# Performance work log

Hardware: AMD Instinct MI355X
Metric: run time of the kernel (lower is better)

Reference implementation:

```python
import jax, jax.numpy as jnp
import numpy as np

N_NODES = 100000
N_EDGES = 1600000
IN_F, HID_F, OUT_F = 128, 128, 128


def setup_inputs() -> dict:
    key = jax.random.key(0)
    k1, k2, k3, k4, k5, k6 = jax.random.split(key, 6)
    x = jax.random.normal(k1, (N_NODES, IN_F), dtype=jnp.float32)
    edge_index = jax.random.randint(k2, (2, N_EDGES), 0, N_NODES, dtype=jnp.int32)
    # nn.Linear params (PyTorch layout: W [out, in], y = x @ W.T + b)
    s1 = 1.0 / np.sqrt(IN_F)
    W1 = jax.random.uniform(k3, (HID_F, IN_F), minval=-s1, maxval=s1, dtype=jnp.float32)
    b1 = jax.random.uniform(k4, (HID_F,), minval=-s1, maxval=s1, dtype=jnp.float32)
    s2 = 1.0 / np.sqrt(HID_F)
    W2 = jax.random.uniform(k5, (OUT_F, HID_F), minval=-s2, maxval=s2, dtype=jnp.float32)
    b2 = jax.random.uniform(k6, (OUT_F,), minval=-s2, maxval=s2, dtype=jnp.float32)
    return {"x": x, "edge_index": edge_index, "W1": W1, "b1": b1, "W2": W2, "b2": b2}


def _spmm_mean(h, row, col, deg_inv):
    # (adj @ h)[i] = sum_{edges e: row[e]==i} h[col[e]], then scale by deg_inv[i]
    agg = jax.ops.segment_sum(h[col], row, num_segments=N_NODES)
    return agg * deg_inv[:, None]


def reference(x, edge_index, W1, b1, W2, b2):
    row, col = edge_index[0], edge_index[1]
    # degree = row-sum of adjacency (duplicates in COO are summed, matching torch)
    deg = jax.ops.segment_sum(jnp.ones((N_EDGES,), dtype=x.dtype), row, num_segments=N_NODES)
    deg_inv = jnp.where(deg > 0, 1.0 / deg, 0.0)
    # dropout in eval mode = identity
    h = x @ W1.T + b1
    h = _spmm_mean(h, row, col, deg_inv)
    h = jax.nn.elu(h)
    h = h @ W2.T + b2
    h = _spmm_mean(h, row, col, deg_inv)
    return h
```

## Files before the change

kernel.cpp:

```cpp
#include <hip/hip_runtime.h>
#include <math.h>

#define N_NODES 100000
#define N_EDGES 1600000
#define F 128
#define NBUCK 196
#define EPB 4096
#define CAP 9216

typedef _Float16 f16x2 __attribute__((ext_vector_type(2)));
typedef _Float16 f16x8 __attribute__((ext_vector_type(8)));
typedef __fp16 fp16x2 __attribute__((ext_vector_type(2)));
typedef float f32x2 __attribute__((ext_vector_type(2)));
typedef float f32x4 __attribute__((ext_vector_type(4)));

__device__ inline uint pkrtz(float a, float b) {
    union { fp16x2 h; uint u; } c;
    c.h = __builtin_amdgcn_cvt_pkrtz(a, b);
    return c.u;
}
__device__ inline f16x2 as2(uint u) {
    union { uint u; f16x2 h; } c; c.u = u; return c.h;
}

__device__ inline int wave_incl_scan(int v, int lane) {
#pragma unroll
    for (int off = 1; off < 64; off <<= 1) {
        int t = __shfl_up(v, off);
        if (lane >= off) v += t;
    }
    return v;
}


__global__ __launch_bounds__(256) void bucketize_kernel(const int* __restrict__ row,
                                                        const int* __restrict__ col,
                                                        int* __restrict__ bucket_cursor,
                                                        int* __restrict__ pairs) {
    __shared__ int stage[EPB];
    __shared__ unsigned char bid[EPB];
    __shared__ int lcnt[NBUCK], lcur[NBUCK], loff[NBUCK], gbase[NBUCK];
    __shared__ int wsum[4];
    const int tid = threadIdx.x;
    const int lane = tid & 63;
    const int wid = tid >> 6;
    const int base = blockIdx.x * EPB;
    const int cnt = min(N_EDGES - base, EPB);

    for (int i = tid; i < NBUCK; i += 256) { lcnt[i] = 0; lcur[i] = 0; }
    __syncthreads();
    for (int i = 0; i < EPB / 256; ++i) {
        int e = base + i * 256 + tid;
        if (e < N_EDGES) atomicAdd(&lcnt[row[e] >> 9], 1);
    }
    __syncthreads();
    {
        int v = (tid < NBUCK) ? lcnt[tid] : 0;
        int inc = wave_incl_scan(v, lane);
        if (lane == 63) wsum[wid] = inc;
        __syncthreads();
        if (tid == 0) {
            int a = 0;
#pragma unroll
            for (int i = 0; i < 4; ++i) { int t = wsum[i]; wsum[i] = a; a += t; }
        }
        __syncthreads();
        if (tid < NBUCK) loff[tid] = inc - v + wsum[wid];
    }
    if (tid < NBUCK) {
        int c = lcnt[tid];
        gbase[tid] = c ? atomicAdd(&bucket_cursor[tid], c) : 0;
    }
    __syncthreads();
    for (int i = 0; i < EPB / 256; ++i) {
        int e = base + i * 256 + tid;
        if (e < N_EDGES) {
            int r = row[e], c = col[e];
            int b = r >> 9;
            int rk = atomicAdd(&lcur[b], 1);
            int q = loff[b] + rk;
            stage[q] = ((r & 511) << 17) | c;
            bid[q] = (unsigned char)b;
        }
    }
    __syncthreads();
    for (int q = tid; q < cnt; q += 256) {
        int b = bid[q];
        int t = gbase[b] + (q - loff[b]);
        if (t < CAP) pairs[b * CAP + t] = stage[q];
    }
}

__global__ __launch_bounds__(512) void csr_finalize_kernel(const int* __restrict__ pairs,
                                                           const int* __restrict__ bucket_cursor,
                                                           int* __restrict__ csr_col,
                                                           int2* __restrict__ rs,
                                                           float* __restrict__ deg_inv) {
    __shared__ int rcnt[512], rcnt2[512], roff[512];
    __shared__ int colstage[CAP];
    __shared__ int wsum[8];
    const int tid = threadIdx.x;
    const int lane = tid & 63;
    const int wid = tid >> 6;
    const int b = blockIdx.x;
    const int cnt = min(bucket_cursor[b], CAP);
    const int base = b * CAP;
    const int* reg = &pairs[base];

    rcnt[tid] = 0;
    rcnt2[tid] = 0;
    __syncthreads();
    for (int q = tid; q < cnt; q += 512) atomicAdd(&rcnt[reg[q] >> 17], 1);
    __syncthreads();
    const int d = rcnt[tid];
    int inc = wave_incl_scan(d, lane);
    if (lane == 63) wsum[wid] = inc;
    __syncthreads();
    if (tid == 0) {
        int a = 0;
#pragma unroll
        for (int i = 0; i < 8; ++i) { int t = wsum[i]; wsum[i] = a; a += t; }
    }
    __syncthreads();
    const int excl = inc - d + wsum[wid];
    roff[tid] = excl;
    const int grow = (b << 9) + tid;
    if (grow < N_NODES) {
        rs[grow] = make_int2(base + excl, d);
        deg_inv[grow] = d ? 1.0f / (float)d : 0.0f;
    }
    __syncthreads();
    for (int q = tid; q < cnt; q += 512) {
        int v = reg[q];
        int lr = v >> 17;
        int rk = atomicAdd(&rcnt2[lr], 1);
        colstage[roff[lr] + rk] = v & 0x1FFFF;
    }
    __syncthreads();
    for (int q = tid; q < cnt; q += 512) csr_col[base + q] = colstage[q];
}


__global__ __launch_bounds__(256) void convert_w_kernel(const float* __restrict__ W1,
                                                        const float* __restrict__ W2,
                                                        uint* __restrict__ W1h,
                                                        uint* __restrict__ W2h) {
    int i = blockIdx.x * 256 + threadIdx.x;
    if (i < F * F / 2) {
        float2 a = *(const float2*)&W1[i * 2];
        float2 b = *(const float2*)&W2[i * 2];
        W1h[i] = pkrtz(a.x, a.y);
        W2h[i] = pkrtz(b.x, b.y);
    }
}


template <bool IN_F16>
__global__ __launch_bounds__(256, 4) void gemm_mfma_kernel(const void* __restrict__ Xv,
                                                           const ushort* __restrict__ Wh,
                                                           const float* __restrict__ bias,
                                                           ushort* __restrict__ Y) {
    __shared__ __align__(16) char smraw[4 * 16 * 132 * 4];
    ushort* xs = (ushort*)smraw;
    float (*ys)[16][132] = (float(*)[16][132])smraw;

    const int tid = threadIdx.x;
    const int m0 = blockIdx.x << 6;

    if (!IN_F16) {
        const float* X = (const float*)Xv;
        for (int i = 0; i < 8; ++i) {
            int f = i * 256 + tid;
            int r = f >> 5, c = f & 31;
            int gr = m0 + r; gr = gr < N_NODES ? gr : N_NODES - 1;
            float4 v = *(const float4*)&X[(size_t)gr * F + (c << 2)];
            uint2 o = {pkrtz(v.x, v.y), pkrtz(v.z, v.w)};
            *(uint2*)&xs[r * 136 + (c << 2)] = o;
        }
    } else {
        const ushort* X = (const ushort*)Xv;
        for (int i = 0; i < 4; ++i) {
            int f = i * 256 + tid;
            int r = f >> 4, c = f & 15;
            int gr = m0 + r; gr = gr < N_NODES ? gr : N_NODES - 1;
            uint4 v = *(const uint4*)&X[(size_t)gr * F + (c << 3)];
            *(uint4*)&xs[r * 136 + (c << 3)] = v;
        }
    }
    __syncthreads();

    const int w = tid >> 6;
    const int lane = tid & 63;
    const int q = lane >> 4;
    const int t = lane & 15;

    f16x8 afr[4];
#pragma unroll
    for (int kk = 0; kk < 4; ++kk)
        afr[kk] = *(const f16x8*)&xs[(w * 16 + t) * 136 + kk * 32 + q * 8];

    f32x4 acc[8];
#pragma unroll
    for (int j = 0; j < 8; ++j) acc[j] = (f32x4){0.f, 0.f, 0.f, 0.f};

#pragma unroll
    for (int j = 0; j < 8; ++j) {
        const ushort* wrow = &Wh[(j * 16 + t) * F + q * 8];
#pragma unroll
        for (int kk = 0; kk < 4; ++kk) {
            f16x8 bfr = *(const f16x8*)&wrow[kk * 32];
            acc[j] = __builtin_amdgcn_mfma_f32_16x16x32_f16(afr[kk], bfr, acc[j], 0, 0, 0);
        }
    }

    __syncthreads();

#pragma unroll
    for (int j = 0; j < 8; ++j) {
        float bb = bias[j * 16 + t];
#pragma unroll
        for (int r = 0; r < 4; ++r) ys[w][q * 4 + r][j * 16 + t] = acc[j][r] + bb;
    }

    for (int i = 0; i < 4; ++i) {
        int c = i * 64 + lane;
        int row = c >> 4, seg = c & 15;
        int gr = m0 + w * 16 + row;
        if (gr < N_NODES) {
            const float* src = &ys[w][row][seg * 8];
            float4 a = *(const float4*)src;
            float4 b = *(const float4*)(src + 4);
            uint4 o = {pkrtz(a.x, a.y), pkrtz(a.z, a.w), pkrtz(b.x, b.y), pkrtz(b.z, b.w)};
            *(uint4*)&Y[(size_t)gr * F + seg * 8] = o;
        }
    }
}


template <bool ELU, bool OUT_F32>
__global__ __launch_bounds__(256) void spmm_kernel(const ushort* __restrict__ H,
                                                   const int2* __restrict__ rs,
                                                   const int* __restrict__ csr_col,
                                                   const float* __restrict__ deg_inv,
                                                   void* __restrict__ out) {
    const int node = blockIdx.x * 16 + (threadIdx.x >> 4);
    const int fo = (threadIdx.x & 15) << 3;

    const int2 sd = rs[node];
    const int s = sd.x;
    const int e = s + sd.y;

    f32x2 a[4];
#pragma unroll
    for (int i = 0; i < 4; ++i) a[i] = (f32x2){0.f, 0.f};

    int p = s;
    while (p + 3 < e) {
        int c0 = csr_col[p], c1 = csr_col[p + 1], c2 = csr_col[p + 2], c3 = csr_col[p + 3];
        uint4 v0 = *(const uint4*)&H[(size_t)c0 * F + fo];
        uint4 v1 = *(const uint4*)&H[(size_t)c1 * F + fo];
        uint4 v2 = *(const uint4*)&H[(size_t)c2 * F + fo];
        uint4 v3 = *(const uint4*)&H[(size_t)c3 * F + fo];
        f16x2 h0 = (as2(v0.x) + as2(v1.x)) + (as2(v2.x) + as2(v3.x));
        f16x2 h1 = (as2(v0.y) + as2(v1.y)) + (as2(v2.y) + as2(v3.y));
        f16x2 h2 = (as2(v0.z) + as2(v1.z)) + (as2(v2.z) + as2(v3.z));
        f16x2 h3 = (as2(v0.w) + as2(v1.w)) + (as2(v2.w) + as2(v3.w));
        a[0] += (f32x2){(float)h0.x, (float)h0.y};
        a[1] += (f32x2){(float)h1.x, (float)h1.y};
        a[2] += (f32x2){(float)h2.x, (float)h2.y};
        a[3] += (f32x2){(float)h3.x, (float)h3.y};
        p += 4;
    }
    if (p + 1 < e) {
        int c0 = csr_col[p], c1 = csr_col[p + 1];
        uint4 v0 = *(const uint4*)&H[(size_t)c0 * F + fo];
        uint4 v1 = *(const uint4*)&H[(size_t)c1 * F + fo];
        f16x2 h0 = as2(v0.x) + as2(v1.x);
        f16x2 h1 = as2(v0.y) + as2(v1.y);
        f16x2 h2 = as2(v0.z) + as2(v1.z);
        f16x2 h3 = as2(v0.w) + as2(v1.w);
        a[0] += (f32x2){(float)h0.x, (float)h0.y};
        a[1] += (f32x2){(float)h1.x, (float)h1.y};
        a[2] += (f32x2){(float)h2.x, (float)h2.y};
        a[3] += (f32x2){(float)h3.x, (float)h3.y};
        p += 2;
    }
    if (p < e) {
        int c = csr_col[p];
        uint4 v = *(const uint4*)&H[(size_t)c * F + fo];
        f16x2 h0 = as2(v.x), h1 = as2(v.y), h2 = as2(v.z), h3 = as2(v.w);
        a[0] += (f32x2){(float)h0.x, (float)h0.y};
        a[1] += (f32x2){(float)h1.x, (float)h1.y};
        a[2] += (f32x2){(float)h2.x, (float)h2.y};
        a[3] += (f32x2){(float)h3.x, (float)h3.y};
    }

    const float di = deg_inv[node];
    float r[8];
#pragma unroll
    for (int i = 0; i < 4; ++i) { r[2 * i] = a[i].x * di; r[2 * i + 1] = a[i].y * di; }
    if (ELU) {
#pragma unroll
        for (int i = 0; i < 8; ++i) r[i] = (r[i] > 0.f) ? r[i] : expm1f(r[i]);
    }
    if (OUT_F32) {
        float* of = &((float*)out)[(size_t)node * F + fo];
        *(float4*)of = (float4){r[0], r[1], r[2], r[3]};
        *(float4*)(of + 4) = (float4){r[4], r[5], r[6], r[7]};
    } else {
        uint4 o = {pkrtz(r[0], r[1]), pkrtz(r[2], r[3]), pkrtz(r[4], r[5]), pkrtz(r[6], r[7])};
        *(uint4*)&((ushort*)out)[(size_t)node * F + fo] = o;
    }
}


extern "C" void kernel_launch(void* const* d_in, const int* in_sizes, int n_in,
                              void* d_out, int out_size, void* d_ws, size_t ws_size,
                              hipStream_t stream) {
    const float* x  = (const float*)d_in[0];
    const int*   ei = (const int*)d_in[1];
    const float* W1 = (const float*)d_in[2];
    const float* b1 = (const float*)d_in[3];
    const float* W2 = (const float*)d_in[4];
    const float* b2 = (const float*)d_in[5];
    float* out = (float*)d_out;

    const int* row = ei;
    const int* col = ei + N_EDGES;

    ushort* bufA = (ushort*)d_ws;
    ushort* bufB = bufA + (size_t)N_NODES * F;
    int* csr_col = (int*)(bufB + (size_t)N_NODES * F);
    int2* rs = (int2*)(csr_col + NBUCK * CAP);
    float* deg_inv = (float*)(rs + N_NODES + 4);
    int* bucket_cursor = (int*)(deg_inv + N_NODES);
    uint* W1h = (uint*)(bucket_cursor + 256);
    uint* W2h = W1h + F * F / 2;
    int* pairs = (int*)bufA;

    (void)hipMemsetAsync(bucket_cursor, 0, NBUCK * sizeof(int), stream);
    bucketize_kernel<<<(N_EDGES + EPB - 1) / EPB, 256, 0, stream>>>(row, col, bucket_cursor, pairs);
    csr_finalize_kernel<<<NBUCK, 512, 0, stream>>>(pairs, bucket_cursor, csr_col, rs, deg_inv);

    convert_w_kernel<<<32, 256, 0, stream>>>(W1, W2, W1h, W2h);

    const int gemm_blocks = (N_NODES + 63) / 64;
    gemm_mfma_kernel<false><<<gemm_blocks, 256, 0, stream>>>(x, (const ushort*)W1h, b1, bufA);
    spmm_kernel<true, false><<<N_NODES / 16, 256, 0, stream>>>(bufA, rs, csr_col, deg_inv, bufB);
    gemm_mfma_kernel<true><<<gemm_blocks, 256, 0, stream>>>(bufB, (const ushort*)W2h, b2, bufA);
    spmm_kernel<false, true><<<N_NODES / 16, 256, 0, stream>>>(bufA, rs, csr_col, deg_inv, out);
}
```

Baseline: 321.3 us.

## Reorder aggregation before GEMM and fuse SpMM with MFMA GEMM per layer

The code uses linearity, A(XW+b) = (AX)W + b·[deg>0], to run the neighbor mean-aggregation first and then the MFMA GEMM inside one fused kernel per layer, with ELU applied in the GEMM epilogue. It drops the separate SpMM kernels and the fp16 intermediate write and read between GEMM and SpMM. A new pass converts x to fp16 up front, and the gather loop is unrolled to 8 edges per step with nontemporal index loads. The catch is that each 16-thread group now gathers 4 nodes in sequence before the GEMM, which cuts the memory-level parallelism available for the latency-bound gather.

```diff
diff --git a/kernel.cpp b/kernel.cpp
--- a/kernel.cpp
+++ b/kernel.cpp
@@ -154,40 +154,112 @@
     }
 }
 
-
-template <bool IN_F16>
-__global__ __launch_bounds__(256, 4) void gemm_mfma_kernel(const void* __restrict__ Xv,
-                                                           const ushort* __restrict__ Wh,
-                                                           const float* __restrict__ bias,
-                                                           ushort* __restrict__ Y) {
+__global__ __launch_bounds__(256) void convert_x_kernel(const float* __restrict__ X,
+                                                        uint* __restrict__ Xh) {
+    int i = blockIdx.x * 256 + threadIdx.x;
+    if (i < N_NODES * F / 8) {
+        float4 a = *(const float4*)&X[(size_t)i * 8];
+        float4 b = *(const float4*)&X[(size_t)i * 8 + 4];
+        uint4 o = {pkrtz(a.x, a.y), pkrtz(a.z, a.w), pkrtz(b.x, b.y), pkrtz(b.z, b.w)};
+        *(uint4*)&Xh[(size_t)i * 4] = o;
+    }
+}
+
+
+template <bool ELU, bool OUT_F32>
+__global__ __launch_bounds__(256, 4) void fused_agg_gemm_kernel(
+        const ushort* __restrict__ H,
+        const int2* __restrict__ rs,
+        const int* __restrict__ csr_col,
+        const float* __restrict__ deg_inv,
+        const ushort* __restrict__ Wh,
+        const float* __restrict__ bias,
+        void* __restrict__ out) {
     __shared__ __align__(16) char smraw[4 * 16 * 132 * 4];
     ushort* xs = (ushort*)smraw;
     float (*ys)[16][132] = (float(*)[16][132])smraw;
 
     const int tid = threadIdx.x;
     const int m0 = blockIdx.x << 6;
-
-    if (!IN_F16) {
-        const float* X = (const float*)Xv;
-        for (int i = 0; i < 8; ++i) {
-            int f = i * 256 + tid;
-            int r = f >> 5, c = f & 31;
-            int gr = m0 + r; gr = gr < N_NODES ? gr : N_NODES - 1;
-            float4 v = *(const float4*)&X[(size_t)gr * F + (c << 2)];
-            uint2 o = {pkrtz(v.x, v.y), pkrtz(v.z, v.w)};
-            *(uint2*)&xs[r * 136 + (c << 2)] = o;
-        }
-    } else {
-        const ushort* X = (const ushort*)Xv;
-        for (int i = 0; i < 4; ++i) {
-            int f = i * 256 + tid;
-            int r = f >> 4, c = f & 15;
-            int gr = m0 + r; gr = gr < N_NODES ? gr : N_NODES - 1;
-            uint4 v = *(const uint4*)&X[(size_t)gr * F + (c << 3)];
-            *(uint4*)&xs[r * 136 + (c << 3)] = v;
-        }
-    }
-    __syncthreads();
+    const int qw = tid >> 4;
+    const int fo = (tid & 15) << 3;
+
+    for (int rr = 0; rr < 4; ++rr) {
+        const int rowi = qw * 4 + rr;
+        const int node = m0 + rowi;
+        f32x2 a[4];
+#pragma unroll
+        for (int i = 0; i < 4; ++i) a[i] = (f32x2){0.f, 0.f};
+        float di = 0.f;
+        if (node < N_NODES) {
+            const int2 sd = rs[node];
+            int p = sd.x;
+            const int e = sd.x + sd.y;
+            di = deg_inv[node];
+            while (p + 7 < e) {
+                int cc[8];
+#pragma unroll
+                for (int k = 0; k < 8; ++k) cc[k] = __builtin_nontemporal_load(&csr_col[p + k]);
+                uint4 vv[8];
+#pragma unroll
+                for (int k = 0; k < 8; ++k) vv[k] = *(const uint4*)&H[(size_t)cc[k] * F + fo];
+#pragma unroll
+                for (int k = 0; k < 8; k += 4) {
+                    f16x2 h0 = (as2(vv[k].x) + as2(vv[k + 1].x)) + (as2(vv[k + 2].x) + as2(vv[k + 3].x));
+                    f16x2 h1 = (as2(vv[k].y) + as2(vv[k + 1].y)) + (as2(vv[k + 2].y) + as2(vv[k + 3].y));
+                    f16x2 h2 = (as2(vv[k].z) + as2(vv[k + 1].z)) + (as2(vv[k + 2].z) + as2(vv[k + 3].z));
+                    f16x2 h3 = (as2(vv[k].w) + as2(vv[k + 1].w)) + (as2(vv[k + 2].w) + as2(vv[k + 3].w));
+                    a[0] += (f32x2){(float)h0.x, (float)h0.y};
+                    a[1] += (f32x2){(float)h1.x, (float)h1.y};
+                    a[2] += (f32x2){(float)h2.x, (float)h2.y};
+                    a[3] += (f32x2){(float)h3.x, (float)h3.y};
+                }
+                p += 8;
+            }
+            if (p + 3 < e) {
+                int c0 = csr_col[p], c1 = csr_col[p + 1], c2 = csr_col[p + 2], c3 = csr_col[p + 3];
+                uint4 v0 = *(const uint4*)&H[(size_t)c0 * F + fo];
+                uint4 v1 = *(const uint4*)&H[(size_t)c1 * F + fo];
+                uint4 v2 = *(const uint4*)&H[(size_t)c2 * F + fo];
+                uint4 v3 = *(const uint4*)&H[(size_t)c3 * F + fo];
+                f16x2 h0 = (as2(v0.x) + as2(v1.x)) + (as2(v2.x) + as2(v3.x));
+                f16x2 h1 = (as2(v0.y) + as2(v1.y)) + (as2(v2.y) + as2(v3.y));
+                f16x2 h2 = (as2(v0.z) + as2(v1.z)) + (as2(v2.z) + as2(v3.z));
+                f16x2 h3 = (as2(v0.w) + as2(v1.w)) + (as2(v2.w) + as2(v3.w));
+                a[0] += (f32x2){(float)h0.x, (float)h0.y};
+                a[1] += (f32x2){(float)h1.x, (float)h1.y};
+                a[2] += (f32x2){(float)h2.x, (float)h2.y};
+                a[3] += (f32x2){(float)h3.x, (float)h3.y};
+                p += 4;
+            }
+            if (p + 1 < e) {
+                int c0 = csr_col[p], c1 = csr_col[p + 1];
+                uint4 v0 = *(const uint4*)&H[(size_t)c0 * F + fo];
+                uint4 v1 = *(const uint4*)&H[(size_t)c1 * F + fo];
+                f16x2 h0 = as2(v0.x) + as2(v1.x);
+                f16x2 h1 = as2(v0.y) + as2(v1.y);
+                f16x2 h2 = as2(v0.z) + as2(v1.z);
+                f16x2 h3 = as2(v0.w) + as2(v1.w);
+                a[0] += (f32x2){(float)h0.x, (float)h0.y};
+                a[1] += (f32x2){(float)h1.x, (float)h1.y};
+                a[2] += (f32x2){(float)h2.x, (float)h2.y};
+                a[3] += (f32x2){(float)h3.x, (float)h3.y};
+                p += 2;
+            }
+            if (p < e) {
+                int c = csr_col[p];
+                uint4 v = *(const uint4*)&H[(size_t)c * F + fo];
+                f16x2 h0 = as2(v.x), h1 = as2(v.y), h2 = as2(v.z), h3 = as2(v.w);
+                a[0] += (f32x2){(float)h0.x, (float)h0.y};
+                a[1] += (f32x2){(float)h1.x, (float)h1.y};
+                a[2] += (f32x2){(float)h2.x, (float)h2.y};
+                a[3] += (f32x2){(float)h3.x, (float)h3.y};
+            }
+        }
+        uint4 o = {pkrtz(a[0].x * di, a[0].y * di), pkrtz(a[1].x * di, a[1].y * di),
+                   pkrtz(a[2].x * di, a[2].y * di), pkrtz(a[3].x * di, a[3].y * di)};
+        *(uint4*)&xs[rowi * 136 + fo] = o;
+    }
 
     const int w = tid >> 6;
     const int lane = tid & 63;
@@ -215,101 +287,40 @@
 
     __syncthreads();
 
+    float mk[4];
+#pragma unroll
+    for (int r = 0; r < 4; ++r) {
+        int gr = m0 + w * 16 + q * 4 + r;
+        int gi = gr < N_NODES ? gr : N_NODES - 1;
+        mk[r] = (gr < N_NODES && deg_inv[gi] > 0.f) ? 1.f : 0.f;
+    }
 #pragma unroll
     for (int j = 0; j < 8; ++j) {
         float bb = bias[j * 16 + t];
 #pragma unroll
-        for (int r = 0; r < 4; ++r) ys[w][q * 4 + r][j * 16 + t] = acc[j][r] + bb;
-    }
-
+        for (int r = 0; r < 4; ++r) {
+            float v = acc[j][r] + bb * mk[r];
+            if (ELU) v = (v > 0.f) ? v : expm1f(v);
+            ys[w][q * 4 + r][j * 16 + t] = v;
+        }
+    }
     for (int i = 0; i < 4; ++i) {
         int c = i * 64 + lane;
-        int row = c >> 4, seg = c & 15;
-        int gr = m0 + w * 16 + row;
+        int rowo = c >> 4, seg = c & 15;
+        int gr = m0 + w * 16 + rowo;
         if (gr < N_NODES) {
-            const float* src = &ys[w][row][seg * 8];
-            float4 a = *(const float4*)src;
-            float4 b = *(const float4*)(src + 4);
-            uint4 o = {pkrtz(a.x, a.y), pkrtz(a.z, a.w), pkrtz(b.x, b.y), pkrtz(b.z, b.w)};
-            *(uint4*)&Y[(size_t)gr * F + seg * 8] = o;
-        }
-    }
-}
-
-
-template <bool ELU, bool OUT_F32>
-__global__ __launch_bounds__(256) void spmm_kernel(const ushort* __restrict__ H,
-                                                   const int2* __restrict__ rs,
-                                                   const int* __restrict__ csr_col,
-                                                   const float* __restrict__ deg_inv,
-                                                   void* __restrict__ out) {
-    const int node = blockIdx.x * 16 + (threadIdx.x >> 4);
-    const int fo = (threadIdx.x & 15) << 3;
-
-    const int2 sd = rs[node];
-    const int s = sd.x;
-    const int e = s + sd.y;
-
-    f32x2 a[4];
-#pragma unroll
-    for (int i = 0; i < 4; ++i) a[i] = (f32x2){0.f, 0.f};
-
-    int p = s;
-    while (p + 3 < e) {
-        int c0 = csr_col[p], c1 = csr_col[p + 1], c2 = csr_col[p + 2], c3 = csr_col[p + 3];
-        uint4 v0 = *(const uint4*)&H[(size_t)c0 * F + fo];
-        uint4 v1 = *(const uint4*)&H[(size_t)c1 * F + fo];
-        uint4 v2 = *(const uint4*)&H[(size_t)c2 * F + fo];
-        uint4 v3 = *(const uint4*)&H[(size_t)c3 * F + fo];
-        f16x2 h0 = (as2(v0.x) + as2(v1.x)) + (as2(v2.x) + as2(v3.x));
-        f16x2 h1 = (as2(v0.y) + as2(v1.y)) + (as2(v2.y) + as2(v3.y));
-        f16x2 h2 = (as2(v0.z) + as2(v1.z)) + (as2(v2.z) + as2(v3.z));
-        f16x2 h3 = (as2(v0.w) + as2(v1.w)) + (as2(v2.w) + as2(v3.w));
-        a[0] += (f32x2){(float)h0.x, (float)h0.y};
-        a[1] += (f32x2){(float)h1.x, (float)h1.y};
-        a[2] += (f32x2){(float)h2.x, (float)h2.y};
-        a[3] += (f32x2){(float)h3.x, (float)h3.y};
-        p += 4;
-    }
-    if (p + 1 < e) {
-        int c0 = csr_col[p], c1 = csr_col[p + 1];
-        uint4 v0 = *(const uint4*)&H[(size_t)c0 * F + fo];
-        uint4 v1 = *(const uint4*)&H[(size_t)c1 * F + fo];
-        f16x2 h0 = as2(v0.x) + as2(v1.x);
-        f16x2 h1 = as2(v0.y) + as2(v1.y);
-        f16x2 h2 = as2(v0.z) + as2(v1.z);
-        f16x2 h3 = as2(v0.w) + as2(v1.w);
-        a[0] += (f32x2){(float)h0.x, (float)h0.y};
-        a[1] += (f32x2){(float)h1.x, (float)h1.y};
-        a[2] += (f32x2){(float)h2.x, (float)h2.y};
-        a[3] += (f32x2){(float)h3.x, (float)h3.y};
-        p += 2;
-    }
-    if (p < e) {
-        int c = csr_col[p];
-        uint4 v = *(const uint4*)&H[(size_t)c * F + fo];
-        f16x2 h0 = as2(v.x), h1 = as2(v.y), h2 = as2(v.z), h3 = as2(v.w);
-        a[0] += (f32x2){(float)h0.x, (float)h0.y};
-        a[1] += (f32x2){(float)h1.x, (float)h1.y};
-        a[2] += (f32x2){(float)h2.x, (float)h2.y};
-        a[3] += (f32x2){(float)h3.x, (float)h3.y};
-    }
-
-    const float di = deg_inv[node];
-    float r[8];
-#pragma unroll
-    for (int i = 0; i < 4; ++i) { r[2 * i] = a[i].x * di; r[2 * i + 1] = a[i].y * di; }
-    if (ELU) {
-#pragma unroll
-        for (int i = 0; i < 8; ++i) r[i] = (r[i] > 0.f) ? r[i] : expm1f(r[i]);
-    }
-    if (OUT_F32) {
-        float* of = &((float*)out)[(size_t)node * F + fo];
-        *(float4*)of = (float4){r[0], r[1], r[2], r[3]};
-        *(float4*)(of + 4) = (float4){r[4], r[5], r[6], r[7]};
-    } else {
-        uint4 o = {pkrtz(r[0], r[1]), pkrtz(r[2], r[3]), pkrtz(r[4], r[5]), pkrtz(r[6], r[7])};
-        *(uint4*)&((ushort*)out)[(size_t)node * F + fo] = o;
+            const float* src = &ys[w][rowo][seg * 8];
+            f32x4 a4 = *(const f32x4*)src;
+            f32x4 b4 = *(const f32x4*)(src + 4);
+            if (OUT_F32) {
+                float* of = &((float*)out)[(size_t)gr * F + seg * 8];
+                __builtin_nontemporal_store(a4, (f32x4*)of);
+                __builtin_nontemporal_store(b4, (f32x4*)(of + 4));
+            } else {
+                uint4 o = {pkrtz(a4.x, a4.y), pkrtz(a4.z, a4.w), pkrtz(b4.x, b4.y), pkrtz(b4.z, b4.w)};
+                *(uint4*)&((ushort*)out)[(size_t)gr * F + seg * 8] = o;
+            }
+        }
     }
 }
 
@@ -343,10 +354,11 @@
     csr_finalize_kernel<<<NBUCK, 512, 0, stream>>>(pairs, bucket_cursor, csr_col, rs, deg_inv);
 
     convert_w_kernel<<<32, 256, 0, stream>>>(W1, W2, W1h, W2h);
-
-    const int gemm_blocks = (N_NODES + 63) / 64;
-    gemm_mfma_kernel<false><<<gemm_blocks, 256, 0, stream>>>(x, (const ushort*)W1h, b1, bufA);
-    spmm_kernel<true, false><<<N_NODES / 16, 256, 0, stream>>>(bufA, rs, csr_col, deg_inv, bufB);
-    gemm_mfma_kernel<true><<<gemm_blocks, 256, 0, stream>>>(bufB, (const ushort*)W2h, b2, bufA);
-    spmm_kernel<false, true><<<N_NODES / 16, 256, 0, stream>>>(bufA, rs, csr_col, deg_inv, out);
-}
+    convert_x_kernel<<<N_NODES * F / 8 / 256, 256, 0, stream>>>(x, (uint*)bufB);
+
+    const int fb = (N_NODES + 63) / 64;
+    fused_agg_gemm_kernel<true, false><<<fb, 256, 0, stream>>>(
+        (const ushort*)bufB, rs, csr_col, deg_inv, (const ushort*)W1h, b1, bufA);
+    fused_agg_gemm_kernel<false, true><<<fb, 256, 0, stream>>>(
+        bufA, rs, csr_col, deg_inv, (const ushort*)W2h, b2, out);
+}
```

Result: slower. 341.6 us (+6.3%).
